# Performance work log

Hardware: AMD Instinct MI355X
Metric: run time of the kernel (lower is better)

The kernel has to match this reference:

```python
import jax, jax.numpy as jnp
import numpy as np

BN_EPS = 1e-5

def _gcn_conv(x, W, b, src, dst, norm, n_nodes):
    # PyG GCNConv: h = x @ W, then out[dst] += norm_e * h[src] (self-loops included in src/dst), + bias
    h = x @ W                                   # [N, F_out]
    msg = h[src] * norm[:, None]                # [E+N, F_out] gather + scale
    out = jax.ops.segment_sum(msg, dst, num_segments=n_nodes)
    return out + b

def _batchnorm(x, gamma, beta):
    # training-mode BN over node axis (biased variance, as torch normalizes with)
    mu = jnp.mean(x, axis=0)
    var = jnp.mean((x - mu) ** 2, axis=0)
    return gamma * (x - mu) * jax.lax.rsqrt(var + BN_EPS) + beta

def setup_inputs() -> dict:
    key = jax.random.key(0)
    ks = jax.random.split(key, 8)
    N, E, Din, H = 100000, 1600000, 128, 128
    x = jax.random.normal(ks[0], (N, Din), dtype=jnp.float32)
    edge_index = jax.random.randint(ks[1], (2, E), 0, N, dtype=jnp.int64)
    def glorot(k, shape):
        lim = float(np.sqrt(6.0 / (shape[0] + shape[1])))
        return jax.random.uniform(k, shape, jnp.float32, -lim, lim)
    return {
        "x": x, "edge_index": edge_index,
        "W1": glorot(ks[2], (Din, H)), "b1": jnp.zeros((H,), jnp.float32),
        "g1": jnp.ones((H,), jnp.float32), "be1": jnp.zeros((H,), jnp.float32),
        "W2": glorot(ks[3], (H, H // 2)), "b2": jnp.zeros((H // 2,), jnp.float32),
        "g2": jnp.ones((H // 2,), jnp.float32), "be2": jnp.zeros((H // 2,), jnp.float32),
        "Wf": glorot(ks[4], (H // 2, 2)), "bf": jnp.zeros((2,), jnp.float32),
    }

def reference(x, edge_index, W1, b1, g1, be1, W2, b2, g2, be2, Wf, bf):
    N = x.shape[0]
    loops = jnp.arange(N, dtype=edge_index.dtype)
    src = jnp.concatenate([edge_index[0], loops])   # add self-loops
    dst = jnp.concatenate([edge_index[1], loops])
    # symmetric GCN normalization: deg from A + I (unit edge weights)
    deg = jax.ops.segment_sum(jnp.ones_like(dst, dtype=x.dtype), dst, num_segments=N)
    dinv = jax.lax.rsqrt(deg)                       # deg >= 1 thanks to self-loops
    norm = dinv[src] * dinv[dst]                    # [E+N]

    h = _gcn_conv(x, W1, b1, src, dst, norm, N)
    h = jax.nn.relu(_batchnorm(h, g1, be1))
    h = _gcn_conv(h, W2, b2, src, dst, norm, N)
    h = jax.nn.relu(_batchnorm(h, g2, be2))
    return h @ Wf + bf                              # [N, 2] logits
```

## Files before the change

### kernel.cpp

```cpp
#include <hip/hip_runtime.h>
#include <hip/hip_fp16.h>
#include <cstdint>
#include <cstddef>

#define BN_EPS 1e-5f
#define NBLK 1024

typedef _Float16 f16x8 __attribute__((ext_vector_type(8)));
typedef float f32x4 __attribute__((ext_vector_type(4)));

__global__ __launch_bounds__(256) void k_flag(const int* __restrict__ e, int* __restrict__ flag, int nSamples) {
    __shared__ int acc;
    if (threadIdx.x == 0) acc = 0;
    __syncthreads();
    int v = 0;
    for (int i = threadIdx.x; i < nSamples; i += 256) v |= e[2 * i + 1];
    atomicOr(&acc, v);
    __syncthreads();
    if (threadIdx.x == 0) *flag = (acc == 0) ? 1 : 0;
}

__device__ __forceinline__ int ld_src(const int* e, int E, int i, int is64) {
    return is64 ? e[2 * i] : e[i];
}
__device__ __forceinline__ int ld_dst(const int* e, int E, int i, int is64) {
    return is64 ? e[2 * (E + i)] : e[E + i];
}

__global__ __launch_bounds__(256) void k_init(float* __restrict__ stats1, float* __restrict__ stats2) {
    int i = threadIdx.x;
    if (i < 256) stats1[i] = 0.0f;
    if (i < 128) stats2[i] = 0.0f;
}

__global__ __launch_bounds__(256) void k_bcount(const int* __restrict__ e, const int* __restrict__ flag,
                                                int* __restrict__ cntMat, int E, int nbC) {
    __shared__ int c[512];
    const int t = threadIdx.x, blk = blockIdx.x;
    for (int b = t; b < nbC; b += 256) c[b] = 0;
    __syncthreads();
    const int is64 = *flag;
    const int chunk = (E + NBLK - 1) / NBLK;
    const int e0 = blk * chunk;
    const int e1 = min(E, e0 + chunk);
    for (int i = e0 + t; i < e1; i += 256) {
        int d = ld_dst(e, E, i, is64);
        atomicAdd(&c[d >> 9], 1);
    }
    __syncthreads();
    for (int b = t; b < nbC; b += 256) cntMat[b * NBLK + blk] = c[b];
}

__global__ __launch_bounds__(256) void k_scan1(const int* __restrict__ in, int* __restrict__ outp,
                                               int* __restrict__ blockSums, int M) {
    __shared__ int sh[256];
    const int t = threadIdx.x;
    const int base = blockIdx.x * 1024 + t * 4;
    int v[4];
#pragma unroll
    for (int i = 0; i < 4; ++i) v[i] = (base + i < M) ? in[base + i] : 0;
    int tot = v[0] + v[1] + v[2] + v[3];
    sh[t] = tot;
    __syncthreads();
    int val = tot;
    for (int o = 1; o < 256; o <<= 1) {
        int x = (t >= o) ? sh[t - o] : 0;
        __syncthreads();
        val += x;
        sh[t] = val;
        __syncthreads();
    }
    int run = val - tot;
#pragma unroll
    for (int i = 0; i < 4; ++i) {
        if (base + i < M) outp[base + i] = run;
        run += v[i];
    }
    if (t == 255) blockSums[blockIdx.x] = val;
}

__global__ __launch_bounds__(256) void k_scan2(int* __restrict__ blockSums, int nB) {
    __shared__ int sh[256];
    const int t = threadIdx.x;
    const int base = t * 4;
    int v[4];
#pragma unroll
    for (int i = 0; i < 4; ++i) v[i] = (base + i < nB) ? blockSums[base + i] : 0;
    int tot = v[0] + v[1] + v[2] + v[3];
    sh[t] = tot;
    __syncthreads();
    int val = tot;
    for (int o = 1; o < 256; o <<= 1) {
        int x = (t >= o) ? sh[t - o] : 0;
        __syncthreads();
        val += x;
        sh[t] = val;
        __syncthreads();
    }
    int run = val - tot;
#pragma unroll
    for (int i = 0; i < 4; ++i) {
        if (base + i < nB) blockSums[base + i] = run;
        run += v[i];
    }
}

__global__ __launch_bounds__(256) void k_scan3(int* __restrict__ outp, const int* __restrict__ blockSums, int M) {
    const int t = threadIdx.x;
    const int off = blockSums[blockIdx.x];
    const int base = blockIdx.x * 1024 + t * 4;
#pragma unroll
    for (int i = 0; i < 4; ++i) {
        int idx = base + i;
        if (idx < M) outp[idx] += off;
    }
}

__global__ __launch_bounds__(256) void k_bscatter(const int* __restrict__ e, const int* __restrict__ flag,
                                                  const int* __restrict__ ofsMat, unsigned* __restrict__ pairBuf,
                                                  int E, int nbC) {
    __shared__ int ofs[512];
    const int t = threadIdx.x, blk = blockIdx.x;
    for (int b = t; b < nbC; b += 256) ofs[b] = ofsMat[b * NBLK + blk];
    __syncthreads();
    const int is64 = *flag;
    const int chunk = (E + NBLK - 1) / NBLK;
    const int e0 = blk * chunk;
    const int e1 = min(E, e0 + chunk);
    for (int i = e0 + t; i < e1; i += 256) {
        int s = ld_src(e, E, i, is64);
        int d = ld_dst(e, E, i, is64);
        int pos = atomicAdd(&ofs[d >> 9], 1);
        pairBuf[pos] = ((unsigned)(d & 511) << 23) | (unsigned)s;
    }
}

__global__ __launch_bounds__(256) void k_fsort(const unsigned* __restrict__ pairBuf, const int* __restrict__ ofsMat,
                                               int* __restrict__ csrSrc, int* __restrict__ rowPtr,
                                               int* __restrict__ cnt, float* __restrict__ dinv,
                                               int E, int N, int nbC) {
    __shared__ int hist[512];
    __shared__ int lofs[512];
    __shared__ int sc[256];
    const int t = threadIdx.x, b = blockIdx.x;
    const int lo = ofsMat[b * NBLK];
    const int hi = (b + 1 < nbC) ? ofsMat[(b + 1) * NBLK] : E;
    hist[t] = 0; hist[t + 256] = 0;
    __syncthreads();
    for (int i = lo + t; i < hi; i += 256) atomicAdd(&hist[pairBuf[i] >> 23], 1);
    __syncthreads();
    int v0 = hist[2 * t], v1 = hist[2 * t + 1];
    int tot = v0 + v1;
    sc[t] = tot;
    __syncthreads();
    int val = tot;
    for (int o = 1; o < 256; o <<= 1) {
        int x = (t >= o) ? sc[t - o] : 0;
        __syncthreads();
        val += x;
        sc[t] = val;
        __syncthreads();
    }
    int excl = val - tot;
    const int d0 = b * 512 + 2 * t;
    const int d1 = d0 + 1;
    lofs[2 * t] = lo + excl;
    lofs[2 * t + 1] = lo + excl + v0;
    if (d0 < N) { rowPtr[d0] = lo + excl;      cnt[d0] = v0; dinv[d0] = rsqrtf((float)(v0 + 1)); }
    if (d1 < N) { rowPtr[d1] = lo + excl + v0; cnt[d1] = v1; dinv[d1] = rsqrtf((float)(v1 + 1)); }
    __syncthreads();
    for (int i = lo + t; i < hi; i += 256) {
        unsigned p = pairBuf[i];
        int dL = p >> 23;
        int s = (int)(p & 0x7FFFFFu);
        int pos = atomicAdd(&lofs[dL], 1);
        csrSrc[pos] = s;
    }
}

__global__ __launch_bounds__(256, 2) void k_gemm1(const float* __restrict__ x, const float* __restrict__ W,
                                                  const float* __restrict__ dinv,
                                                  _Float16* __restrict__ hs1, int N) {
    __shared__ _Float16 Ws[128][136];
    __shared__ _Float16 xs[128][136];
    const int t = threadIdx.x;
    const int row0 = blockIdx.x * 128;

#pragma unroll
    for (int i = 0; i < 16; ++i) {
        int j = t + i * 256;
        int k = j >> 5, c = (j & 31) << 2;
        float4 v = ((const float4*)W)[j];
        union { _Float16 h[4]; uint2 u; } p;
        p.h[0] = (_Float16)v.x; p.h[1] = (_Float16)v.y; p.h[2] = (_Float16)v.z; p.h[3] = (_Float16)v.w;
        *(uint2*)&Ws[k][c] = p.u;
    }
#pragma unroll
    for (int i = 0; i < 16; ++i) {
        int j = t + i * 256;
        int r = j >> 5, c = (j & 31) << 2;
        int gr = row0 + r;
        float4 v = make_float4(0.f, 0.f, 0.f, 0.f);
        if (gr < N) v = *(const float4*)&x[(size_t)gr * 128 + c];
        union { _Float16 h[4]; uint2 u; } p;
        p.h[0] = (_Float16)v.x; p.h[1] = (_Float16)v.y; p.h[2] = (_Float16)v.z; p.h[3] = (_Float16)v.w;
        *(uint2*)&xs[r][c] = p.u;
    }
    __syncthreads();

    const int w = t >> 6, l = t & 63;
    const int wm = w >> 1, wn = w & 1;
    const int l15 = l & 15, lg = l >> 4;

    f16x8 bfr[4][4];
#pragma unroll
    for (int nt = 0; nt < 4; ++nt)
#pragma unroll
        for (int ks = 0; ks < 4; ++ks) {
            int col = wn * 64 + nt * 16 + l15;
            int kb = ks * 32 + lg * 8;
            f16x8 b;
#pragma unroll
            for (int j = 0; j < 8; ++j) b[j] = Ws[kb + j][col];
            bfr[nt][ks] = b;
        }

    f32x4 acc[4][4];
#pragma unroll
    for (int mt = 0; mt < 4; ++mt)
#pragma unroll
        for (int nt = 0; nt < 4; ++nt) acc[mt][nt] = (f32x4)(0.f);

#pragma unroll
    for (int mt = 0; mt < 4; ++mt) {
        const int r = wm * 64 + mt * 16 + l15;
        f16x8 afr[4];
#pragma unroll
        for (int ks = 0; ks < 4; ++ks) afr[ks] = *(const f16x8*)&xs[r][ks * 32 + lg * 8];
#pragma unroll
        for (int nt = 0; nt < 4; ++nt)
#pragma unroll
            for (int ks = 0; ks < 4; ++ks)
                acc[mt][nt] = __builtin_amdgcn_mfma_f32_16x16x32_f16(afr[ks], bfr[nt][ks], acc[mt][nt], 0, 0, 0);
    }

#pragma unroll
    for (int mt = 0; mt < 4; ++mt) {
        const int rbase = row0 + wm * 64 + mt * 16 + lg * 4;
#pragma unroll
        for (int rr = 0; rr < 4; ++rr) {
            int gr = rbase + rr;
            if (gr < N) {
                float dv = dinv[gr];
#pragma unroll
                for (int nt = 0; nt < 4; ++nt) {
                    int col = wn * 64 + nt * 16 + l15;
                    hs1[(size_t)gr * 128 + col] = (_Float16)(acc[mt][nt][rr] * dv);
                }
            }
        }
    }
}

__global__ __launch_bounds__(256) void k_gather128(const int* __restrict__ csrSrc, const int* __restrict__ rowPtr,
                                                   const int* __restrict__ cnt, const float* __restrict__ dinv,
                                                   const __half2* __restrict__ hs, float* __restrict__ agg, int N) {
    int wave = (blockIdx.x * 256 + threadIdx.x) >> 6;
    int lane = threadIdx.x & 63;
    if (wave >= N) return;
    const int d = wave;
    float2 acc = __half22float2(hs[(size_t)d * 64 + lane]);
    const int start = rowPtr[d];
    const int c = cnt[d];
    const int* __restrict__ p = csrSrc + start;
    int j = 0;
    for (; j + 3 < c; j += 4) {
        int s0 = p[j], s1 = p[j + 1], s2 = p[j + 2], s3 = p[j + 3];
        float2 v0 = __half22float2(hs[(size_t)s0 * 64 + lane]);
        float2 v1 = __half22float2(hs[(size_t)s1 * 64 + lane]);
        float2 v2 = __half22float2(hs[(size_t)s2 * 64 + lane]);
        float2 v3 = __half22float2(hs[(size_t)s3 * 64 + lane]);
        acc.x += (v0.x + v1.x) + (v2.x + v3.x);
        acc.y += (v0.y + v1.y) + (v2.y + v3.y);
    }
    for (; j < c; ++j) {
        float2 v = __half22float2(hs[(size_t)p[j] * 64 + lane]);
        acc.x += v.x;
        acc.y += v.y;
    }
    const float wgt = dinv[d];
    acc.x *= wgt; acc.y *= wgt;
    *(float2*)&agg[(size_t)d * 128 + lane * 2] = acc;
}

__global__ __launch_bounds__(256) void k_gather64(const int* __restrict__ csrSrc, const int* __restrict__ rowPtr,
                                                  const int* __restrict__ cnt, const float* __restrict__ dinv,
                                                  const __half* __restrict__ hs, float* __restrict__ agg, int N) {
    int wave = (blockIdx.x * 256 + threadIdx.x) >> 6;
    int lane = threadIdx.x & 63;
    if (wave >= N) return;
    const int d = wave;
    float acc = __half2float(hs[(size_t)d * 64 + lane]);
    const int start = rowPtr[d];
    const int c = cnt[d];
    const int* __restrict__ p = csrSrc + start;
    int j = 0;
    for (; j + 3 < c; j += 4) {
        int s0 = p[j], s1 = p[j + 1], s2 = p[j + 2], s3 = p[j + 3];
        float v0 = __half2float(hs[(size_t)s0 * 64 + lane]);
        float v1 = __half2float(hs[(size_t)s1 * 64 + lane]);
        float v2 = __half2float(hs[(size_t)s2 * 64 + lane]);
        float v3 = __half2float(hs[(size_t)s3 * 64 + lane]);
        acc += (v0 + v1) + (v2 + v3);
    }
    for (; j < c; ++j) acc += __half2float(hs[(size_t)p[j] * 64 + lane]);
    agg[(size_t)d * 64 + lane] = acc * dinv[d];
}

template <int F>
__global__ __launch_bounds__(256) void k_stats(const float* __restrict__ a, float* __restrict__ stats, int N) {
    const int t = threadIdx.x;
    const int f = t & (F - 1);
    const int sub = t / F;
    const int rpb = 256 / F;
    float s = 0.f, s2 = 0.f;
    for (int r = blockIdx.x * rpb + sub; r < N; r += gridDim.x * rpb) {
        float v = a[(size_t)r * F + f];
        s += v;
        s2 += v * v;
    }
    __shared__ float ls[256], ls2[256];
    ls[t] = s; ls2[t] = s2;
    __syncthreads();
    if (t < F) {
#pragma unroll
        for (int i = 1; i < rpb; ++i) { s += ls[t + i * F]; s2 += ls2[t + i * F]; }
        atomicAdd(&stats[f], s);
        atomicAdd(&stats[F + f], s2);
    }
}

__global__ void k_bnparam(const float* __restrict__ stats, const float* __restrict__ g, const float* __restrict__ be,
                          float* __restrict__ ss, int N, int F) {
    int f = threadIdx.x;
    if (f < F) {
        float invN = 1.0f / (float)N;
        float mean = stats[f] * invN;
        float var = stats[F + f] * invN - mean * mean;
        var = fmaxf(var, 0.f);
        float inv = rsqrtf(var + BN_EPS);
        float scale = g[f] * inv;
        ss[f] = scale;
        ss[F + f] = be[f] - mean * scale;
    }
}

__global__ __launch_bounds__(256, 2) void k_gemm2(const float* __restrict__ a_in, const float* __restrict__ W,
                                                  const float* __restrict__ ss, const float* __restrict__ dinv,
                                                  _Float16* __restrict__ hs2, int N) {
    __shared__ _Float16 Ws[128][72];
    __shared__ _Float16 xs[128][136];
    const int t = threadIdx.x;
    const int row0 = blockIdx.x * 128;

#pragma unroll
    for (int i = 0; i < 8; ++i) {
        int j = t + i * 256;
        int k = j >> 4, c = (j & 15) << 2;
        float4 v = ((const float4*)W)[j];
        union { _Float16 h[4]; uint2 u; } p;
        p.h[0] = (_Float16)v.x; p.h[1] = (_Float16)v.y; p.h[2] = (_Float16)v.z; p.h[3] = (_Float16)v.w;
        *(uint2*)&Ws[k][c] = p.u;
    }
#pragma unroll
    for (int i = 0; i < 16; ++i) {
        int j = t + i * 256;
        int r = j >> 5, c = (j & 31) << 2;
        int gr = row0 + r;
        float4 v = make_float4(0.f, 0.f, 0.f, 0.f);
        if (gr < N) {
            v = *(const float4*)&a_in[(size_t)gr * 128 + c];
            float4 sc = *(const float4*)&ss[c];
            float4 sh = *(const float4*)&ss[128 + c];
            v.x = fmaxf(0.f, fmaf(v.x, sc.x, sh.x));
            v.y = fmaxf(0.f, fmaf(v.y, sc.y, sh.y));
            v.z = fmaxf(0.f, fmaf(v.z, sc.z, sh.z));
            v.w = fmaxf(0.f, fmaf(v.w, sc.w, sh.w));
        }
        union { _Float16 h[4]; uint2 u; } p;
        p.h[0] = (_Float16)v.x; p.h[1] = (_Float16)v.y; p.h[2] = (_Float16)v.z; p.h[3] = (_Float16)v.w;
        *(uint2*)&xs[r][c] = p.u;
    }
    __syncthreads();

    const int w = t >> 6, l = t & 63;
    const int wm = w >> 1, wn = w & 1;
    const int l15 = l & 15, lg = l >> 4;

    f16x8 bfr[2][4];
#pragma unroll
    for (int nt = 0; nt < 2; ++nt)
#pragma unroll
        for (int ks = 0; ks < 4; ++ks) {
            int col = wn * 32 + nt * 16 + l15;
            int kb = ks * 32 + lg * 8;
            f16x8 b;
#pragma unroll
            for (int j = 0; j < 8; ++j) b[j] = Ws[kb + j][col];
            bfr[nt][ks] = b;
        }

    f32x4 acc[4][2];
#pragma unroll
    for (int mt = 0; mt < 4; ++mt)
#pragma unroll
        for (int nt = 0; nt < 2; ++nt) acc[mt][nt] = (f32x4)(0.f);

#pragma unroll
    for (int mt = 0; mt < 4; ++mt) {
        const int r = wm * 64 + mt * 16 + l15;
        f16x8 afr[4];
#pragma unroll
        for (int ks = 0; ks < 4; ++ks) afr[ks] = *(const f16x8*)&xs[r][ks * 32 + lg * 8];
#pragma unroll
        for (int nt = 0; nt < 2; ++nt)
#pragma unroll
            for (int ks = 0; ks < 4; ++ks)
                acc[mt][nt] = __builtin_amdgcn_mfma_f32_16x16x32_f16(afr[ks], bfr[nt][ks], acc[mt][nt], 0, 0, 0);
    }

#pragma unroll
    for (int mt = 0; mt < 4; ++mt) {
        const int rbase = row0 + wm * 64 + mt * 16 + lg * 4;
#pragma unroll
        for (int rr = 0; rr < 4; ++rr) {
            int gr = rbase + rr;
            if (gr < N) {
                float dv = dinv[gr];
#pragma unroll
                for (int nt = 0; nt < 2; ++nt) {
                    int col = wn * 32 + nt * 16 + l15;
                    hs2[(size_t)gr * 64 + col] = (_Float16)(acc[mt][nt][rr] * dv);
                }
            }
        }
    }
}

__global__ __launch_bounds__(256) void k_final(const float* __restrict__ a_in, const float* __restrict__ ss,
                                               const float* __restrict__ Wf, const float* __restrict__ bf,
                                               float* __restrict__ out, int N) {
    __shared__ float buf[256][65];
    const int t = threadIdx.x;
    const int row0 = blockIdx.x * 256;

#pragma unroll
    for (int i = 0; i < 16; ++i) {
        int j = t + i * 256;
        int r = j >> 4;
        int k = (j & 15) << 2;
        float4 v = make_float4(0.f, 0.f, 0.f, 0.f);
        int gr = row0 + r;
        if (gr < N) {
            v = *(const float4*)&a_in[(size_t)gr * 64 + k];
            float4 sc = *(const float4*)&ss[k];
            float4 sh = *(const float4*)&ss[64 + k];
            v.x = fmaxf(0.f, fmaf(v.x, sc.x, sh.x));
            v.y = fmaxf(0.f, fmaf(v.y, sc.y, sh.y));
            v.z = fmaxf(0.f, fmaf(v.z, sc.z, sh.z));
            v.w = fmaxf(0.f, fmaf(v.w, sc.w, sh.w));
        }
        buf[r][k + 0] = v.x; buf[r][k + 1] = v.y; buf[r][k + 2] = v.z; buf[r][k + 3] = v.w;
    }
    __syncthreads();

    int gr = row0 + t;
    if (gr < N) {
        float a0 = 0.f, a1 = 0.f;
        for (int k = 0; k < 64; ++k) {
            float v = buf[t][k];
            a0 = fmaf(v, Wf[2 * k + 0], a0);
            a1 = fmaf(v, Wf[2 * k + 1], a1);
        }
        out[(size_t)gr * 2 + 0] = a0 + bf[0];
        out[(size_t)gr * 2 + 1] = a1 + bf[1];
    }
}

extern "C" void kernel_launch(void* const* d_in, const int* in_sizes, int n_in,
                              void* d_out, int out_size, void* d_ws, size_t ws_size,
                              hipStream_t stream) {
    const float* x   = (const float*)d_in[0];
    const int*   ei  = (const int*)d_in[1];
    const float* W1  = (const float*)d_in[2];
    const float* g1  = (const float*)d_in[4];
    const float* be1 = (const float*)d_in[5];
    const float* W2  = (const float*)d_in[6];
    const float* g2  = (const float*)d_in[8];
    const float* be2 = (const float*)d_in[9];
    const float* Wf  = (const float*)d_in[10];
    const float* bf  = (const float*)d_in[11];
    float* out = (float*)d_out;

    const int N = in_sizes[0] / 128;
    const int E = in_sizes[1] / 2;
    const int nbC = (N + 511) >> 9;
    const int M = nbC * NBLK;
    const int nBs = (M + 1023) / 1024;

    float* fws = (float*)d_ws;
    int*   flag   = (int*)fws;
    float* stats1 = fws + 64;
    float* stats2 = fws + 320;
    float* ss1    = fws + 448;
    float* ss2    = fws + 704;
    int*   blockSums = (int*)(fws + 832);

    const size_t Na = (size_t)((N + 255) & ~255);
    const size_t Ea = (size_t)((E + 255) & ~255);
    const size_t Ma = (size_t)((M + 255) & ~255);
    size_t off = 2048;
    int*   cnt    = (int*)(fws + off);  off += Na;
    int*   rowPtr = (int*)(fws + off);  off += Na;
    float* dinv   = fws + off;          off += Na;
    int*   cntMat = (int*)(fws + off);  off += Ma;
    int*   ofsMat = (int*)(fws + off);  off += Ma;
    int*   csrSrc = (int*)(fws + off);  off += Ea;
    _Float16* hs1 = (_Float16*)(fws + off);
    float* agg1   = fws + off + (size_t)N * 64;
    _Float16* hs2 = hs1;
    float* agg2   = agg1;
    unsigned* pairBuf = (unsigned*)hs1;

    int nSamp = E < 65536 ? E : 65536;

    k_flag<<<1, 256, 0, stream>>>(ei, flag, nSamp);
    k_init<<<1, 256, 0, stream>>>(stats1, stats2);

    k_bcount<<<NBLK, 256, 0, stream>>>(ei, flag, cntMat, E, nbC);
    k_scan1<<<nBs, 256, 0, stream>>>(cntMat, ofsMat, blockSums, M);
    k_scan2<<<1, 256, 0, stream>>>(blockSums, nBs);
    k_scan3<<<nBs, 256, 0, stream>>>(ofsMat, blockSums, M);
    k_bscatter<<<NBLK, 256, 0, stream>>>(ei, flag, ofsMat, pairBuf, E, nbC);
    k_fsort<<<nbC, 256, 0, stream>>>(pairBuf, ofsMat, csrSrc, rowPtr, cnt, dinv, E, N, nbC);

    k_gemm1<<<(N + 127) / 128, 256, 0, stream>>>(x, W1, dinv, hs1, N);
    k_gather128<<<(N * 64 + 255) / 256, 256, 0, stream>>>(csrSrc, rowPtr, cnt, dinv,
                                                          (const __half2*)hs1, agg1, N);
    k_stats<128><<<512, 256, 0, stream>>>(agg1, stats1, N);
    k_bnparam<<<1, 128, 0, stream>>>(stats1, g1, be1, ss1, N, 128);

    k_gemm2<<<(N + 127) / 128, 256, 0, stream>>>(agg1, W2, ss1, dinv, hs2, N);
    k_gather64<<<(N * 64 + 255) / 256, 256, 0, stream>>>(csrSrc, rowPtr, cnt, dinv,
                                                         (const __half*)hs2, agg2, N);
    k_stats<64><<<512, 256, 0, stream>>>(agg2, stats2, N);
    k_bnparam<<<1, 128, 0, stream>>>(stats2, g2, be2, ss2, N, 64);

    k_final<<<(N + 255) / 256, 256, 0, stream>>>(agg2, ss2, Wf, bf, out, N);
}
```

Baseline: 355.0 us.

## Store aggregation outputs in fp16, unroll gathers by 8, merge init kernel

The aggregation buffers after each gather are now written as fp16 instead of fp32, and the stats, gemm2 and final kernels read them as half. This roughly halves the bytes moved between the gather and its consumer kernels. The gather loops are unrolled to 8 and use readfirstlane to make row indices scalar, which exposes more memory-level parallelism. The stats-zeroing kernel is folded into the flag kernel and NBLK is cut from 1024 to 256. The cost is fp16 rounding of pre-BatchNorm activations, which adds precision risk, especially in the sum-of-squares statistics.

```diff
diff --git a/kernel.cpp b/kernel.cpp
--- a/kernel.cpp
+++ b/kernel.cpp
@@ -4,18 +4,21 @@
 #include <cstddef>
 
 #define BN_EPS 1e-5f
-#define NBLK 1024
+#define NBLK 256
 
 typedef _Float16 f16x8 __attribute__((ext_vector_type(8)));
 typedef float f32x4 __attribute__((ext_vector_type(4)));
 
-__global__ __launch_bounds__(256) void k_flag(const int* __restrict__ e, int* __restrict__ flag, int nSamples) {
+__global__ __launch_bounds__(256) void k_flag(const int* __restrict__ e, int* __restrict__ flag, int nSamples,
+                                              float* __restrict__ stats1, float* __restrict__ stats2) {
     __shared__ int acc;
     if (threadIdx.x == 0) acc = 0;
     __syncthreads();
     int v = 0;
     for (int i = threadIdx.x; i < nSamples; i += 256) v |= e[2 * i + 1];
     atomicOr(&acc, v);
+    if (threadIdx.x < 256) stats1[threadIdx.x] = 0.0f;
+    if (threadIdx.x < 128) stats2[threadIdx.x] = 0.0f;
     __syncthreads();
     if (threadIdx.x == 0) *flag = (acc == 0) ? 1 : 0;
 }
@@ -25,12 +28,6 @@
 }
 __device__ __forceinline__ int ld_dst(const int* e, int E, int i, int is64) {
     return is64 ? e[2 * (E + i)] : e[E + i];
-}
-
-__global__ __launch_bounds__(256) void k_init(float* __restrict__ stats1, float* __restrict__ stats2) {
-    int i = threadIdx.x;
-    if (i < 256) stats1[i] = 0.0f;
-    if (i < 128) stats2[i] = 0.0f;
 }
 
 __global__ __launch_bounds__(256) void k_bcount(const int* __restrict__ e, const int* __restrict__ flag,
@@ -264,79 +261,96 @@
 
 __global__ __launch_bounds__(256) void k_gather128(const int* __restrict__ csrSrc, const int* __restrict__ rowPtr,
                                                    const int* __restrict__ cnt, const float* __restrict__ dinv,
-                                                   const __half2* __restrict__ hs, float* __restrict__ agg, int N) {
-    int wave = (blockIdx.x * 256 + threadIdx.x) >> 6;
-    int lane = threadIdx.x & 63;
-    if (wave >= N) return;
-    const int d = wave;
-    float2 acc = __half22float2(hs[(size_t)d * 64 + lane]);
-    const int start = rowPtr[d];
-    const int c = cnt[d];
+                                                   const __half2* __restrict__ hs, __half2* __restrict__ agg, int N) {
+    int wv = (blockIdx.x * 256 + threadIdx.x) >> 6;
+    if (wv >= N) return;
+    const int d = __builtin_amdgcn_readfirstlane(wv);
+    const int lane = threadIdx.x & 63;
+    const size_t fo = (size_t)d * 64 + lane;
+    float2 acc = __half22float2(hs[fo]);
+    const int start = __builtin_amdgcn_readfirstlane(rowPtr[d]);
+    const int c = __builtin_amdgcn_readfirstlane(cnt[d]);
     const int* __restrict__ p = csrSrc + start;
     int j = 0;
+    for (; j + 7 < c; j += 8) {
+        float2 v[8];
+#pragma unroll
+        for (int u = 0; u < 8; ++u) v[u] = __half22float2(hs[(size_t)p[j + u] * 64 + lane]);
+#pragma unroll
+        for (int u = 0; u < 8; ++u) { acc.x += v[u].x; acc.y += v[u].y; }
+    }
     for (; j + 3 < c; j += 4) {
-        int s0 = p[j], s1 = p[j + 1], s2 = p[j + 2], s3 = p[j + 3];
-        float2 v0 = __half22float2(hs[(size_t)s0 * 64 + lane]);
-        float2 v1 = __half22float2(hs[(size_t)s1 * 64 + lane]);
-        float2 v2 = __half22float2(hs[(size_t)s2 * 64 + lane]);
-        float2 v3 = __half22float2(hs[(size_t)s3 * 64 + lane]);
-        acc.x += (v0.x + v1.x) + (v2.x + v3.x);
-        acc.y += (v0.y + v1.y) + (v2.y + v3.y);
+        float2 v[4];
+#pragma unroll
+        for (int u = 0; u < 4; ++u) v[u] = __half22float2(hs[(size_t)p[j + u] * 64 + lane]);
+#pragma unroll
+        for (int u = 0; u < 4; ++u) { acc.x += v[u].x; acc.y += v[u].y; }
     }
     for (; j < c; ++j) {
         float2 v = __half22float2(hs[(size_t)p[j] * 64 + lane]);
-        acc.x += v.x;
-        acc.y += v.y;
+        acc.x += v.x; acc.y += v.y;
     }
     const float wgt = dinv[d];
-    acc.x *= wgt; acc.y *= wgt;
-    *(float2*)&agg[(size_t)d * 128 + lane * 2] = acc;
+    agg[fo] = __floats2half2_rn(acc.x * wgt, acc.y * wgt);
 }
 
 __global__ __launch_bounds__(256) void k_gather64(const int* __restrict__ csrSrc, const int* __restrict__ rowPtr,
                                                   const int* __restrict__ cnt, const float* __restrict__ dinv,
-                                                  const __half* __restrict__ hs, float* __restrict__ agg, int N) {
-    int wave = (blockIdx.x * 256 + threadIdx.x) >> 6;
-    int lane = threadIdx.x & 63;
-    if (wave >= N) return;
-    const int d = wave;
-    float acc = __half2float(hs[(size_t)d * 64 + lane]);
-    const int start = rowPtr[d];
-    const int c = cnt[d];
+                                                  const __half* __restrict__ hs, __half* __restrict__ agg, int N) {
+    int wv = (blockIdx.x * 256 + threadIdx.x) >> 6;
+    if (wv >= N) return;
+    const int d = __builtin_amdgcn_readfirstlane(wv);
+    const int lane = threadIdx.x & 63;
+    const size_t fo = (size_t)d * 64 + lane;
+    float acc = __half2float(hs[fo]);
+    const int start = __builtin_amdgcn_readfirstlane(rowPtr[d]);
+    const int c = __builtin_amdgcn_readfirstlane(cnt[d]);
     const int* __restrict__ p = csrSrc + start;
     int j = 0;
+    for (; j + 7 < c; j += 8) {
+        float v[8];
+#pragma unroll
+        for (int u = 0; u < 8; ++u) v[u] = __half2float(hs[(size_t)p[j + u] * 64 + lane]);
+#pragma unroll
+        for (int u = 0; u < 8; ++u) acc += v[u];
+    }
     for (; j + 3 < c; j += 4) {
-        int s0 = p[j], s1 = p[j + 1], s2 = p[j + 2], s3 = p[j + 3];
-        float v0 = __half2float(hs[(size_t)s0 * 64 + lane]);
-        float v1 = __half2float(hs[(size_t)s1 * 64 + lane]);
-        float v2 = __half2float(hs[(size_t)s2 * 64 + lane]);
-        float v3 = __half2float(hs[(size_t)s3 * 64 + lane]);
-        acc += (v0 + v1) + (v2 + v3);
+        float v[4];
+#pragma unroll
+        for (int u = 0; u < 4; ++u) v[u] = __half2float(hs[(size_t)p[j + u] * 64 + lane]);
+#pragma unroll
+        for (int u = 0; u < 4; ++u) acc += v[u];
     }
     for (; j < c; ++j) acc += __half2float(hs[(size_t)p[j] * 64 + lane]);
-    agg[(size_t)d * 64 + lane] = acc * dinv[d];
+    agg[fo] = __float2half(acc * dinv[d]);
 }
 
 template <int F>
-__global__ __launch_bounds__(256) void k_stats(const float* __restrict__ a, float* __restrict__ stats, int N) {
-    const int t = threadIdx.x;
-    const int f = t & (F - 1);
-    const int sub = t / F;
-    const int rpb = 256 / F;
-    float s = 0.f, s2 = 0.f;
+__global__ __launch_bounds__(256) void k_stats_h(const __half2* __restrict__ a, float* __restrict__ stats, int N) {
+    const int S = F / 2;
+    const int t = threadIdx.x;
+    const int slot = t & (S - 1);
+    const int sub = t / S;
+    const int rpb = 256 / S;
+    float sx = 0.f, sy = 0.f, qx = 0.f, qy = 0.f;
     for (int r = blockIdx.x * rpb + sub; r < N; r += gridDim.x * rpb) {
-        float v = a[(size_t)r * F + f];
-        s += v;
-        s2 += v * v;
-    }
-    __shared__ float ls[256], ls2[256];
-    ls[t] = s; ls2[t] = s2;
-    __syncthreads();
-    if (t < F) {
-#pragma unroll
-        for (int i = 1; i < rpb; ++i) { s += ls[t + i * F]; s2 += ls2[t + i * F]; }
-        atomicAdd(&stats[f], s);
-        atomicAdd(&stats[F + f], s2);
+        float2 v = __half22float2(a[(size_t)r * S + slot]);
+        sx += v.x; sy += v.y;
+        qx += v.x * v.x; qy += v.y * v.y;
+    }
+    __shared__ float l0[256], l1[256], l2[256], l3[256];
+    l0[t] = sx; l1[t] = sy; l2[t] = qx; l3[t] = qy;
+    __syncthreads();
+    if (t < S) {
+#pragma unroll
+        for (int i = 1; i < rpb; ++i) {
+            sx += l0[t + i * S]; sy += l1[t + i * S];
+            qx += l2[t + i * S]; qy += l3[t + i * S];
+        }
+        atomicAdd(&stats[2 * t], sx);
+        atomicAdd(&stats[2 * t + 1], sy);
+        atomicAdd(&stats[F + 2 * t], qx);
+        atomicAdd(&stats[F + 2 * t + 1], qy);
     }
 }
 
@@ -355,7 +369,7 @@
     }
 }
 
-__global__ __launch_bounds__(256, 2) void k_gemm2(const float* __restrict__ a_in, const float* __restrict__ W,
+__global__ __launch_bounds__(256, 2) void k_gemm2(const __half* __restrict__ a_in, const float* __restrict__ W,
                                                   const float* __restrict__ ss, const float* __restrict__ dinv,
                                                   _Float16* __restrict__ hs2, int N) {
     __shared__ _Float16 Ws[128][72];
@@ -379,13 +393,16 @@
         int gr = row0 + r;
         float4 v = make_float4(0.f, 0.f, 0.f, 0.f);
         if (gr < N) {
-            v = *(const float4*)&a_in[(size_t)gr * 128 + c];
+            union { uint2 u; __half2 h[2]; } iv;
+            iv.u = *(const uint2*)&a_in[(size_t)gr * 128 + c];
+            float2 v01 = __half22float2(iv.h[0]);
+            float2 v23 = __half22float2(iv.h[1]);
             float4 sc = *(const float4*)&ss[c];
             float4 sh = *(const float4*)&ss[128 + c];
-            v.x = fmaxf(0.f, fmaf(v.x, sc.x, sh.x));
-            v.y = fmaxf(0.f, fmaf(v.y, sc.y, sh.y));
-            v.z = fmaxf(0.f, fmaf(v.z, sc.z, sh.z));
-            v.w = fmaxf(0.f, fmaf(v.w, sc.w, sh.w));
+            v.x = fmaxf(0.f, fmaf(v01.x, sc.x, sh.x));
+            v.y = fmaxf(0.f, fmaf(v01.y, sc.y, sh.y));
+            v.z = fmaxf(0.f, fmaf(v23.x, sc.z, sh.z));
+            v.w = fmaxf(0.f, fmaf(v23.y, sc.w, sh.w));
         }
         union { _Float16 h[4]; uint2 u; } p;
         p.h[0] = (_Float16)v.x; p.h[1] = (_Float16)v.y; p.h[2] = (_Float16)v.z; p.h[3] = (_Float16)v.w;
@@ -447,7 +464,7 @@
     }
 }
 
-__global__ __launch_bounds__(256) void k_final(const float* __restrict__ a_in, const float* __restrict__ ss,
+__global__ __launch_bounds__(256) void k_final(const __half* __restrict__ a_in, const float* __restrict__ ss,
                                                const float* __restrict__ Wf, const float* __restrict__ bf,
                                                float* __restrict__ out, int N) {
     __shared__ float buf[256][65];
@@ -462,13 +479,16 @@
         float4 v = make_float4(0.f, 0.f, 0.f, 0.f);
         int gr = row0 + r;
         if (gr < N) {
-            v = *(const float4*)&a_in[(size_t)gr * 64 + k];
+            union { uint2 u; __half2 h[2]; } iv;
+            iv.u = *(const uint2*)&a_in[(size_t)gr * 64 + k];
+            float2 v01 = __half22float2(iv.h[0]);
+            float2 v23 = __half22float2(iv.h[1]);
             float4 sc = *(const float4*)&ss[k];
             float4 sh = *(const float4*)&ss[64 + k];
-            v.x = fmaxf(0.f, fmaf(v.x, sc.x, sh.x));
-            v.y = fmaxf(0.f, fmaf(v.y, sc.y, sh.y));
-            v.z = fmaxf(0.f, fmaf(v.z, sc.z, sh.z));
-            v.w = fmaxf(0.f, fmaf(v.w, sc.w, sh.w));
+            v.x = fmaxf(0.f, fmaf(v01.x, sc.x, sh.x));
+            v.y = fmaxf(0.f, fmaf(v01.y, sc.y, sh.y));
+            v.z = fmaxf(0.f, fmaf(v23.x, sc.z, sh.z));
+            v.w = fmaxf(0.f, fmaf(v23.y, sc.w, sh.w));
         }
         buf[r][k + 0] = v.x; buf[r][k + 1] = v.y; buf[r][k + 2] = v.z; buf[r][k + 3] = v.w;
     }
@@ -527,15 +547,14 @@
     int*   ofsMat = (int*)(fws + off);  off += Ma;
     int*   csrSrc = (int*)(fws + off);  off += Ea;
     _Float16* hs1 = (_Float16*)(fws + off);
-    float* agg1   = fws + off + (size_t)N * 64;
+    __half*  agg1 = (__half*)(fws + off + (size_t)N * 64);
     _Float16* hs2 = hs1;
-    float* agg2   = agg1;
+    __half*  agg2 = agg1;
     unsigned* pairBuf = (unsigned*)hs1;
 
     int nSamp = E < 65536 ? E : 65536;
 
-    k_flag<<<1, 256, 0, stream>>>(ei, flag, nSamp);
-    k_init<<<1, 256, 0, stream>>>(stats1, stats2);
+    k_flag<<<1, 256, 0, stream>>>(ei, flag, nSamp, stats1, stats2);
 
     k_bcount<<<NBLK, 256, 0, stream>>>(ei, flag, cntMat, E, nbC);
     k_scan1<<<nBs, 256, 0, stream>>>(cntMat, ofsMat, blockSums, M);
@@ -546,14 +565,14 @@
 
     k_gemm1<<<(N + 127) / 128, 256, 0, stream>>>(x, W1, dinv, hs1, N);
     k_gather128<<<(N * 64 + 255) / 256, 256, 0, stream>>>(csrSrc, rowPtr, cnt, dinv,
-                                                          (const __half2*)hs1, agg1, N);
-    k_stats<128><<<512, 256, 0, stream>>>(agg1, stats1, N);
+                                                          (const __half2*)hs1, (__half2*)agg1, N);
+    k_stats_h<128><<<512, 256, 0, stream>>>((const __half2*)agg1, stats1, N);
     k_bnparam<<<1, 128, 0, stream>>>(stats1, g1, be1, ss1, N, 128);
 
     k_gemm2<<<(N + 127) / 128, 256, 0, stream>>>(agg1, W2, ss1, dinv, hs2, N);
     k_gather64<<<(N * 64 + 255) / 256, 256, 0, stream>>>(csrSrc, rowPtr, cnt, dinv,
                                                          (const __half*)hs2, agg2, N);
-    k_stats<64><<<512, 256, 0, stream>>>(agg2, stats2, N);
+    k_stats_h<64><<<512, 256, 0, stream>>>((const __half2*)agg2, stats2, N);
     k_bnparam<<<1, 128, 0, stream>>>(stats2, g2, be2, ss2, N, 64);
 
     k_final<<<(N + 255) / 256, 256, 0, stream>>>(agg2, ss2, Wf, bf, out, N);
```

Result: faster. 325.1 us (-8.4%).
